# Optimization experiments

Measured on AMD Instinct MI355X. Metric: run time of the kernel, lower is better.

Reference implementation:

```python
import jax, jax.numpy as jnp
import numpy as np

# Predictive-coding graph message passing (PCGraphConv core compute).
# Single-graph edge list (edge_src -> edge_dst) with one scalar weight per edge,
# tiled over the batch (weights.repeat(1, batchsize) in the original).
# PredictionMessagePassing: mu_i = sum_{e: dst(e)=i} w_e * f(x_{src(e)})
# ValueMessagePassing:      dx_j = -eps_j + f'(x_j) * sum_{e: src(e)=j} w_e * eps_{dst(e)}
# with eps = x - mu and f = tanh.

N_PER_GRAPH = 4096
E_PER_GRAPH = 524288
BATCH = 32


def setup_inputs() -> dict:
    key = jax.random.key(0)
    k1, k2, k3, k4 = jax.random.split(key, 4)
    x = jax.random.normal(k1, (BATCH * N_PER_GRAPH,), dtype=jnp.float32)
    weights = jax.random.normal(k2, (E_PER_GRAPH,), dtype=jnp.float32) * (1.0 / np.sqrt(N_PER_GRAPH))
    edge_src = jax.random.randint(k3, (E_PER_GRAPH,), 0, N_PER_GRAPH, dtype=jnp.int32)
    edge_dst = jax.random.randint(k4, (E_PER_GRAPH,), 0, N_PER_GRAPH, dtype=jnp.int32)
    return {"x": x, "weights": weights, "edge_src": edge_src, "edge_dst": edge_dst,
            "batch_size": BATCH, "num_vertices": N_PER_GRAPH}


def reference(x, weights, edge_src, edge_dst, batch_size, num_vertices):
    B, N = batch_size, num_vertices
    BN = B * N
    # Tile single-graph edges across the batch with per-graph node offsets.
    offs = (jnp.arange(B, dtype=edge_src.dtype) * N)[:, None]        # [B,1]
    src = (edge_src[None, :] + offs).reshape(-1)                     # [B*E]
    dst = (edge_dst[None, :] + offs).reshape(-1)                     # [B*E]
    w = jnp.tile(weights, B)                                         # [B*E]

    fx = jnp.tanh(x)                                                 # f(x)
    # Predictions: gather f(x) at src, weight per edge, scatter-add at dst.
    mu = jax.ops.segment_sum(w * fx[src], dst, num_segments=BN)      # [B*N]
    eps = x - mu                                                     # errors
    fprime = 1.0 - fx * fx                                           # f'(x)
    # Value update: backward flow of errors along edges.
    dx = -eps + fprime * jax.ops.segment_sum(w * eps[dst], src, num_segments=BN)
    return jnp.stack([mu, dx])                                       # [2, B*N]
```

## Files before the change

kernel.cpp:

```cpp
#include <hip/hip_runtime.h>


static constexpr int kB = 32, kLogB = 5;
static constexpr int kTileNodes = 8;
static constexpr int kNumBins = 512;
static constexpr int kCap = 1408;
static constexpr int kChunk = 2048;
static constexpr int kRowPad = 33;

__global__ void __launch_bounds__(256) k_init(
    const float* __restrict__ x, float* __restrict__ x_t,
    float* __restrict__ fx_t, int N) {
  __shared__ float tile[32][65];
  int tid = threadIdx.x;
  int n0 = blockIdx.x * 64;
  for (int k = tid; k < 32 * 64; k += 256) {
    int b = k >> 6, n = k & 63;
    tile[b][n] = x[b * N + n0 + n];
  }
  __syncthreads();
  for (int k = tid; k < 64 * 32; k += 256) {
    int n = k >> 5, b = k & 31;
    float xv = tile[b][n];
    int j = (n0 + n) * kB + b;
    x_t[j] = xv;
    fx_t[j] = tanhf(xv);
  }
}

__global__ void __launch_bounds__(1024) k_bin_dual(
    const int* __restrict__ esrc, const int* __restrict__ edst,
    const float* __restrict__ w, uint2* __restrict__ binsA,
    uint2* __restrict__ binsB, int* __restrict__ cursA,
    int* __restrict__ cursB, int E) {
  __shared__ int histA[kNumBins], histB[kNumBins];
  __shared__ int baseA[kNumBins], baseB[kNumBins];
  int tid = threadIdx.x;
  int e0 = blockIdx.x * kChunk;
  int nloc = min(kChunk, E - e0);
  if (tid < kNumBins) { histA[tid] = 0; histB[tid] = 0; }
  __syncthreads();
  int k0 = tid, k1 = tid + 1024;
  int s0 = 0, d0 = 0, s1 = 0, d1 = 0;
  unsigned lA0 = 0, lB0 = 0, lA1 = 0, lB1 = 0;
  bool has0 = k0 < nloc, has1 = k1 < nloc;
  if (has0) {
    s0 = esrc[e0 + k0]; d0 = edst[e0 + k0];
    lA0 = atomicAdd(&histA[d0 >> 3], 1);
    lB0 = atomicAdd(&histB[s0 >> 3], 1);
  }
  if (has1) {
    s1 = esrc[e0 + k1]; d1 = edst[e0 + k1];
    lA1 = atomicAdd(&histA[d1 >> 3], 1);
    lB1 = atomicAdd(&histB[s1 >> 3], 1);
  }
  __syncthreads();
  if (tid < kNumBins) {
    baseA[tid] = atomicAdd(&cursA[tid], histA[tid]);
    baseB[tid] = atomicAdd(&cursB[tid], histB[tid]);
  }
  __syncthreads();
  if (has0) {
    unsigned wu = __float_as_uint(w[e0 + k0]);
    int binA = d0 >> 3; int posA = baseA[binA] + (int)lA0;
    if (posA < kCap)
      binsA[(size_t)binA * kCap + posA] = make_uint2(((unsigned)s0 << 8) | (d0 & 7), wu);
    int binB = s0 >> 3; int posB = baseB[binB] + (int)lB0;
    if (posB < kCap)
      binsB[(size_t)binB * kCap + posB] = make_uint2(((unsigned)d0 << 8) | (s0 & 7), wu);
  }
  if (has1) {
    unsigned wu = __float_as_uint(w[e0 + k1]);
    int binA = d1 >> 3; int posA = baseA[binA] + (int)lA1;
    if (posA < kCap)
      binsA[(size_t)binA * kCap + posA] = make_uint2(((unsigned)s1 << 8) | (d1 & 7), wu);
    int binB = s1 >> 3; int posB = baseB[binB] + (int)lB1;
    if (posB < kCap)
      binsB[(size_t)binB * kCap + posB] = make_uint2(((unsigned)d1 << 8) | (s1 & 7), wu);
  }
}

__global__ void __launch_bounds__(1024) k_accum(
    const uint2* __restrict__ bins, const int* __restrict__ cursors,
    const float* __restrict__ vals, const float* __restrict__ x_t,
    const float* __restrict__ fx_t, float* __restrict__ eps_t,
    float* __restrict__ out, int N, int mode) {
  __shared__ float acc[32][kTileNodes * kRowPad];
  int tid = threadIdx.x;
  int b = tid & 31;
  int slot = tid >> 5;
  float* my = acc[slot];
#pragma unroll
  for (int l = 0; l < kTileNodes; l++) my[l * kRowPad + b] = 0.0f;
  int t = blockIdx.x;
  int cnt = min(cursors[t], kCap);
  const uint2* bp = bins + (size_t)t * kCap;

  int i = slot;
  uint2 r0 = (i      < cnt) ? bp[i]      : make_uint2(0u, 0u);
  uint2 r1 = (i + 32 < cnt) ? bp[i + 32] : make_uint2(0u, 0u);
  uint2 r2 = (i + 64 < cnt) ? bp[i + 64] : make_uint2(0u, 0u);
  float v0 = (i      < cnt) ? vals[((r0.x >> 8) << kLogB) + b] : 0.0f;
  float v1 = (i + 32 < cnt) ? vals[((r1.x >> 8) << kLogB) + b] : 0.0f;
  while (i < cnt) {
    uint2 r3 = (i + 96 < cnt) ? bp[i + 96] : make_uint2(0u, 0u);
    float v2 = (i + 64 < cnt) ? vals[((r2.x >> 8) << kLogB) + b] : 0.0f;
    my[(r0.x & 7) * kRowPad + b] += __uint_as_float(r0.y) * v0;
    r0 = r1; r1 = r2; r2 = r3; v0 = v1; v1 = v2;
    i += 32;
  }
  __syncthreads();
  if (tid < kTileNodes * kB) {
    int local = tid & 7, bb = tid >> 3;
    float s = 0.0f;
#pragma unroll
    for (int sl = 0; sl < 32; sl++) s += acc[sl][local * kRowPad + bb];
    int n = t * kTileNodes + local;
    int j = n * kB + bb;
    if (mode == 0) {
      out[bb * N + n] = s;
      eps_t[j] = x_t[j] - s;
    } else {
      float fx = fx_t[j];
      out[bb * N + n] = fmaf(1.0f - fx * fx, s, -eps_t[j]);
    }
  }
}

extern "C" void kernel_launch(void* const* d_in, const int* in_sizes, int n_in,
                              void* d_out, int out_size, void* d_ws, size_t ws_size,
                              hipStream_t stream) {
  const float* x    = (const float*)d_in[0];
  const float* w    = (const float*)d_in[1];
  const int*   esrc = (const int*)d_in[2];
  const int*   edst = (const int*)d_in[3];

  const int BN = in_sizes[0];
  const int E  = in_sizes[1];
  const int N  = BN / kB;

  float* ws    = (float*)d_ws;
  float* x_t   = ws;
  float* fx_t  = ws + (size_t)BN;
  float* eps_t = ws + 2 * (size_t)BN;
  int*   cursA = (int*)(ws + 3 * (size_t)BN);
  int*   cursB = cursA + kNumBins;
  uint2* binsA = (uint2*)(cursB + kNumBins);
  uint2* binsB = binsA + (size_t)kNumBins * kCap;

  float* out_mu = (float*)d_out;
  float* out_dx = (float*)d_out + BN;

  int nblk_bin = (E + kChunk - 1) / kChunk;

  hipMemsetAsync(cursA, 0, 2 * kNumBins * sizeof(int), stream);
  k_init<<<N / 64, 256, 0, stream>>>(x, x_t, fx_t, N);
  k_bin_dual<<<nblk_bin, 1024, 0, stream>>>(esrc, edst, w, binsA, binsB,
                                            cursA, cursB, E);
  k_accum<<<kNumBins, 1024, 0, stream>>>(binsA, cursA, fx_t, x_t, fx_t,
                                         eps_t, out_mu, N, 0);
  k_accum<<<kNumBins, 1024, 0, stream>>>(binsB, cursB, eps_t, x_t, fx_t,
                                         eps_t, out_dx, N, 1);
}
```

Baseline: 116.4 us.

## Fuse init, binning and both accumulations into one cooperative persistent kernel

Replaces the memset plus four kernel launches with a single cooperative kernel that uses grid-wide syncs between the init, binning and two accumulation phases. It also halves the block size to 512 threads, using 16 slots with a deeper prefetch pipeline, and moves the cursor zeroing into the kernel. The aim is to remove launch gaps and memset overhead. In exchange it adds grid.sync cost and lowers per-block parallelism in the accumulation. A non-cooperative multi-kernel fallback is kept.

```diff
diff --git a/kernel.cpp b/kernel.cpp
--- a/kernel.cpp
+++ b/kernel.cpp
@@ -1,25 +1,30 @@
 #include <hip/hip_runtime.h>
+#include <hip/hip_cooperative_groups.h>
+
+namespace cg = cooperative_groups;
 
 
 static constexpr int kB = 32, kLogB = 5;
-static constexpr int kTileNodes = 8;
+static constexpr int kT = 8;
 static constexpr int kNumBins = 512;
 static constexpr int kCap = 1408;
-static constexpr int kChunk = 2048;
-static constexpr int kRowPad = 33;
-
-__global__ void __launch_bounds__(256) k_init(
-    const float* __restrict__ x, float* __restrict__ x_t,
-    float* __restrict__ fx_t, int N) {
-  __shared__ float tile[32][65];
+static constexpr int kPad = 36;
+static constexpr int kSlots = 16;
+static constexpr int kChunk = 1024;
+static constexpr int kLdsF = kSlots * kT * kPad;
+
+
+__device__ __forceinline__ void init_tile(float* ldsf, const float* __restrict__ x,
+    float* __restrict__ x_t, float* __restrict__ fx_t, int N, int g) {
+  float (*tile)[65] = (float(*)[65])ldsf;
   int tid = threadIdx.x;
-  int n0 = blockIdx.x * 64;
-  for (int k = tid; k < 32 * 64; k += 256) {
+  int n0 = g * 64;
+  for (int k = tid; k < 32 * 64; k += 512) {
     int b = k >> 6, n = k & 63;
     tile[b][n] = x[b * N + n0 + n];
   }
   __syncthreads();
-  for (int k = tid; k < 64 * 32; k += 256) {
+  for (int k = tid; k < 64 * 32; k += 512) {
     int n = k >> 5, b = k & 31;
     float xv = tile[b][n];
     int j = (n0 + n) * kB + b;
@@ -28,94 +33,88 @@
   }
 }
 
-__global__ void __launch_bounds__(1024) k_bin_dual(
+__device__ __forceinline__ void bin_chunk(float* ldsf,
     const int* __restrict__ esrc, const int* __restrict__ edst,
     const float* __restrict__ w, uint2* __restrict__ binsA,
     uint2* __restrict__ binsB, int* __restrict__ cursA,
-    int* __restrict__ cursB, int E) {
-  __shared__ int histA[kNumBins], histB[kNumBins];
-  __shared__ int baseA[kNumBins], baseB[kNumBins];
+    int* __restrict__ cursB, int E, int c) {
+  int* histA = (int*)ldsf;
+  int* histB = histA + kNumBins;
+  int* baseA = histB + kNumBins;
+  int* baseB = baseA + kNumBins;
   int tid = threadIdx.x;
-  int e0 = blockIdx.x * kChunk;
+  histA[tid] = 0; histB[tid] = 0;
+  __syncthreads();
+  int e0 = c * kChunk;
   int nloc = min(kChunk, E - e0);
-  if (tid < kNumBins) { histA[tid] = 0; histB[tid] = 0; }
-  __syncthreads();
-  int k0 = tid, k1 = tid + 1024;
+  int k0 = tid, k1 = tid + 512;
   int s0 = 0, d0 = 0, s1 = 0, d1 = 0;
-  unsigned lA0 = 0, lB0 = 0, lA1 = 0, lB1 = 0;
-  bool has0 = k0 < nloc, has1 = k1 < nloc;
-  if (has0) {
+  unsigned a0 = 0, b0 = 0, a1 = 0, b1 = 0;
+  bool h0 = k0 < nloc, h1 = k1 < nloc;
+  if (h0) {
     s0 = esrc[e0 + k0]; d0 = edst[e0 + k0];
-    lA0 = atomicAdd(&histA[d0 >> 3], 1);
-    lB0 = atomicAdd(&histB[s0 >> 3], 1);
-  }
-  if (has1) {
+    a0 = atomicAdd(&histA[d0 >> 3], 1);
+    b0 = atomicAdd(&histB[s0 >> 3], 1);
+  }
+  if (h1) {
     s1 = esrc[e0 + k1]; d1 = edst[e0 + k1];
-    lA1 = atomicAdd(&histA[d1 >> 3], 1);
-    lB1 = atomicAdd(&histB[s1 >> 3], 1);
-  }
-  __syncthreads();
-  if (tid < kNumBins) {
-    baseA[tid] = atomicAdd(&cursA[tid], histA[tid]);
-    baseB[tid] = atomicAdd(&cursB[tid], histB[tid]);
-  }
-  __syncthreads();
-  if (has0) {
+    a1 = atomicAdd(&histA[d1 >> 3], 1);
+    b1 = atomicAdd(&histB[s1 >> 3], 1);
+  }
+  __syncthreads();
+  baseA[tid] = atomicAdd(&cursA[tid], histA[tid]);
+  baseB[tid] = atomicAdd(&cursB[tid], histB[tid]);
+  __syncthreads();
+  if (h0) {
     unsigned wu = __float_as_uint(w[e0 + k0]);
-    int binA = d0 >> 3; int posA = baseA[binA] + (int)lA0;
-    if (posA < kCap)
-      binsA[(size_t)binA * kCap + posA] = make_uint2(((unsigned)s0 << 8) | (d0 & 7), wu);
-    int binB = s0 >> 3; int posB = baseB[binB] + (int)lB0;
-    if (posB < kCap)
-      binsB[(size_t)binB * kCap + posB] = make_uint2(((unsigned)d0 << 8) | (s0 & 7), wu);
-  }
-  if (has1) {
+    int bin = d0 >> 3; int p = baseA[bin] + (int)a0;
+    if (p < kCap) binsA[(size_t)bin * kCap + p] = make_uint2(((unsigned)s0 << 8) | (d0 & 7), wu);
+    bin = s0 >> 3; p = baseB[bin] + (int)b0;
+    if (p < kCap) binsB[(size_t)bin * kCap + p] = make_uint2(((unsigned)d0 << 8) | (s0 & 7), wu);
+  }
+  if (h1) {
     unsigned wu = __float_as_uint(w[e0 + k1]);
-    int binA = d1 >> 3; int posA = baseA[binA] + (int)lA1;
-    if (posA < kCap)
-      binsA[(size_t)binA * kCap + posA] = make_uint2(((unsigned)s1 << 8) | (d1 & 7), wu);
-    int binB = s1 >> 3; int posB = baseB[binB] + (int)lB1;
-    if (posB < kCap)
-      binsB[(size_t)binB * kCap + posB] = make_uint2(((unsigned)d1 << 8) | (s1 & 7), wu);
-  }
-}
-
-__global__ void __launch_bounds__(1024) k_accum(
+    int bin = d1 >> 3; int p = baseA[bin] + (int)a1;
+    if (p < kCap) binsA[(size_t)bin * kCap + p] = make_uint2(((unsigned)s1 << 8) | (d1 & 7), wu);
+    bin = s1 >> 3; p = baseB[bin] + (int)b1;
+    if (p < kCap) binsB[(size_t)bin * kCap + p] = make_uint2(((unsigned)d1 << 8) | (s1 & 7), wu);
+  }
+}
+
+__device__ __forceinline__ void accum_bin(float* ldsf,
     const uint2* __restrict__ bins, const int* __restrict__ cursors,
     const float* __restrict__ vals, const float* __restrict__ x_t,
     const float* __restrict__ fx_t, float* __restrict__ eps_t,
-    float* __restrict__ out, int N, int mode) {
-  __shared__ float acc[32][kTileNodes * kRowPad];
-  int tid = threadIdx.x;
-  int b = tid & 31;
-  int slot = tid >> 5;
-  float* my = acc[slot];
+    float* __restrict__ out, int N, int t, int mode) {
+  int tid = threadIdx.x, b = tid & 31, slot = tid >> 5;
+  float* my = ldsf + slot * (kT * kPad);
 #pragma unroll
-  for (int l = 0; l < kTileNodes; l++) my[l * kRowPad + b] = 0.0f;
-  int t = blockIdx.x;
+  for (int l = 0; l < kT; l++) my[l * kPad + b] = 0.0f;
   int cnt = min(cursors[t], kCap);
   const uint2* bp = bins + (size_t)t * kCap;
-
   int i = slot;
   uint2 r0 = (i      < cnt) ? bp[i]      : make_uint2(0u, 0u);
-  uint2 r1 = (i + 32 < cnt) ? bp[i + 32] : make_uint2(0u, 0u);
-  uint2 r2 = (i + 64 < cnt) ? bp[i + 64] : make_uint2(0u, 0u);
+  uint2 r1 = (i + 16 < cnt) ? bp[i + 16] : make_uint2(0u, 0u);
+  uint2 r2 = (i + 32 < cnt) ? bp[i + 32] : make_uint2(0u, 0u);
+  uint2 r3 = (i + 48 < cnt) ? bp[i + 48] : make_uint2(0u, 0u);
   float v0 = (i      < cnt) ? vals[((r0.x >> 8) << kLogB) + b] : 0.0f;
-  float v1 = (i + 32 < cnt) ? vals[((r1.x >> 8) << kLogB) + b] : 0.0f;
+  float v1 = (i + 16 < cnt) ? vals[((r1.x >> 8) << kLogB) + b] : 0.0f;
+  float v2 = (i + 32 < cnt) ? vals[((r2.x >> 8) << kLogB) + b] : 0.0f;
   while (i < cnt) {
-    uint2 r3 = (i + 96 < cnt) ? bp[i + 96] : make_uint2(0u, 0u);
-    float v2 = (i + 64 < cnt) ? vals[((r2.x >> 8) << kLogB) + b] : 0.0f;
-    my[(r0.x & 7) * kRowPad + b] += __uint_as_float(r0.y) * v0;
-    r0 = r1; r1 = r2; r2 = r3; v0 = v1; v1 = v2;
-    i += 32;
-  }
-  __syncthreads();
-  if (tid < kTileNodes * kB) {
+    uint2 r4 = (i + 64 < cnt) ? bp[i + 64] : make_uint2(0u, 0u);
+    float v3 = (i + 48 < cnt) ? vals[((r3.x >> 8) << kLogB) + b] : 0.0f;
+    my[(r0.x & 7) * kPad + b] += __uint_as_float(r0.y) * v0;
+    r0 = r1; r1 = r2; r2 = r3; r3 = r4;
+    v0 = v1; v1 = v2; v2 = v3;
+    i += 16;
+  }
+  __syncthreads();
+  if (tid < kT * kB) {
     int local = tid & 7, bb = tid >> 3;
     float s = 0.0f;
 #pragma unroll
-    for (int sl = 0; sl < 32; sl++) s += acc[sl][local * kRowPad + bb];
-    int n = t * kTileNodes + local;
+    for (int sl = 0; sl < kSlots; sl++) s += ldsf[sl * (kT * kPad) + local * kPad + bb];
+    int n = t * kT + local;
     int j = n * kB + bb;
     if (mode == 0) {
       out[bb * N + n] = s;
@@ -127,6 +126,76 @@
   }
 }
 
+
+__global__ void __launch_bounds__(512, 4) k_fused(
+    const float* __restrict__ x, const float* __restrict__ w,
+    const int* __restrict__ esrc, const int* __restrict__ edst,
+    float* __restrict__ x_t, float* __restrict__ fx_t,
+    float* __restrict__ eps_t, int* __restrict__ cursA,
+    int* __restrict__ cursB, uint2* __restrict__ binsA,
+    uint2* __restrict__ binsB, float* __restrict__ out_mu,
+    float* __restrict__ out_dx, int N, int E) {
+  cg::grid_group grid = cg::this_grid();
+  __shared__ float ldsf[kLdsF];
+  int blk = blockIdx.x, G = gridDim.x, tid = threadIdx.x;
+
+  if (blk == 0 && tid < kNumBins) { cursA[tid] = 0; cursB[tid] = 0; }
+  int nTiles = N >> 6;
+  for (int g = blk; g < nTiles; g += G) {
+    __syncthreads();
+    init_tile(ldsf, x, x_t, fx_t, N, g);
+  }
+  grid.sync();
+
+  int nChunks = (E + kChunk - 1) / kChunk;
+  for (int c = blk; c < nChunks; c += G) {
+    __syncthreads();
+    bin_chunk(ldsf, esrc, edst, w, binsA, binsB, cursA, cursB, E, c);
+  }
+  grid.sync();
+
+  for (int t = blk; t < kNumBins; t += G) {
+    __syncthreads();
+    accum_bin(ldsf, binsA, cursA, fx_t, x_t, fx_t, eps_t, out_mu, N, t, 0);
+  }
+  grid.sync();
+
+  for (int t = blk; t < kNumBins; t += G) {
+    __syncthreads();
+    accum_bin(ldsf, binsB, cursB, eps_t, x_t, fx_t, eps_t, out_dx, N, t, 1);
+  }
+}
+
+
+__global__ void __launch_bounds__(512) k_init(
+    const float* __restrict__ x, float* __restrict__ x_t,
+    float* __restrict__ fx_t, int* __restrict__ cursA,
+    int* __restrict__ cursB, int N) {
+  __shared__ float ldsf[32 * 65];
+  if (blockIdx.x == 0 && threadIdx.x < kNumBins) {
+    cursA[threadIdx.x] = 0; cursB[threadIdx.x] = 0;
+  }
+  init_tile(ldsf, x, x_t, fx_t, N, blockIdx.x);
+}
+
+__global__ void __launch_bounds__(512) k_bin(
+    const int* __restrict__ esrc, const int* __restrict__ edst,
+    const float* __restrict__ w, uint2* __restrict__ binsA,
+    uint2* __restrict__ binsB, int* __restrict__ cursA,
+    int* __restrict__ cursB, int E) {
+  __shared__ float ldsf[4 * kNumBins];
+  bin_chunk(ldsf, esrc, edst, w, binsA, binsB, cursA, cursB, E, blockIdx.x);
+}
+
+__global__ void __launch_bounds__(512) k_accum(
+    const uint2* __restrict__ bins, const int* __restrict__ cursors,
+    const float* __restrict__ vals, const float* __restrict__ x_t,
+    const float* __restrict__ fx_t, float* __restrict__ eps_t,
+    float* __restrict__ out, int N, int mode) {
+  __shared__ float ldsf[kLdsF];
+  accum_bin(ldsf, bins, cursors, vals, x_t, fx_t, eps_t, out, N, blockIdx.x, mode);
+}
+
 extern "C" void kernel_launch(void* const* d_in, const int* in_sizes, int n_in,
                               void* d_out, int out_size, void* d_ws, size_t ws_size,
                               hipStream_t stream) {
@@ -135,9 +204,9 @@
   const int*   esrc = (const int*)d_in[2];
   const int*   edst = (const int*)d_in[3];
 
-  const int BN = in_sizes[0];
-  const int E  = in_sizes[1];
-  const int N  = BN / kB;
+  int BN = in_sizes[0];
+  int E  = in_sizes[1];
+  int N  = BN / kB;
 
   float* ws    = (float*)d_ws;
   float* x_t   = ws;
@@ -151,14 +220,27 @@
   float* out_mu = (float*)d_out;
   float* out_dx = (float*)d_out + BN;
 
-  int nblk_bin = (E + kChunk - 1) / kChunk;
-
-  hipMemsetAsync(cursA, 0, 2 * kNumBins * sizeof(int), stream);
-  k_init<<<N / 64, 256, 0, stream>>>(x, x_t, fx_t, N);
-  k_bin_dual<<<nblk_bin, 1024, 0, stream>>>(esrc, edst, w, binsA, binsB,
-                                            cursA, cursB, E);
-  k_accum<<<kNumBins, 1024, 0, stream>>>(binsA, cursA, fx_t, x_t, fx_t,
-                                         eps_t, out_mu, N, 0);
-  k_accum<<<kNumBins, 1024, 0, stream>>>(binsB, cursB, eps_t, x_t, fx_t,
-                                         eps_t, out_dx, N, 1);
-}
+  int dev = 0; (void)hipGetDevice(&dev);
+  int coop = 0, ncu = 0, nb = 0;
+  (void)hipDeviceGetAttribute(&coop, hipDeviceAttributeCooperativeLaunch, dev);
+  (void)hipDeviceGetAttribute(&ncu, hipDeviceAttributeMultiprocessorCount, dev);
+  (void)hipOccupancyMaxActiveBlocksPerMultiprocessor(&nb, (const void*)k_fused, 512, 0);
+
+  if (coop && (long)nb * (long)ncu >= (long)kNumBins) {
+    void* args[] = {&x, &w, &esrc, &edst, &x_t, &fx_t, &eps_t,
+                    &cursA, &cursB, &binsA, &binsB, &out_mu, &out_dx, &N, &E};
+    hipError_t err = hipLaunchCooperativeKernel((const void*)k_fused,
+                                                dim3(kNumBins), dim3(512),
+                                                args, 0, stream);
+    if (err == hipSuccess) return;
+    (void)hipGetLastError();
+  }
+
+  k_init<<<N / 64, 512, 0, stream>>>(x, x_t, fx_t, cursA, cursB, N);
+  k_bin<<<(E + kChunk - 1) / kChunk, 512, 0, stream>>>(esrc, edst, w, binsA,
+                                                       binsB, cursA, cursB, E);
+  k_accum<<<kNumBins, 512, 0, stream>>>(binsA, cursA, fx_t, x_t, fx_t, eps_t,
+                                        out_mu, N, 0);
+  k_accum<<<kNumBins, 512, 0, stream>>>(binsB, cursB, eps_t, x_t, fx_t, eps_t,
+                                        out_dx, N, 1);
+}
```

New measurement: 331.9 us. +185.2%, slower.
